# Performance work log

Hardware: AMD Instinct MI355X
Metric: run time of the kernel (lower is better)

The kernel has to match this reference:

```python
import jax, jax.numpy as jnp
import numpy as np

B, C, N, DI, DC = 64, 32, 1152, 8, 16
ROUTINGS = 3


def squash(x, axis=-1):
    sq = jnp.sum(x * x, axis=axis, keepdims=True)
    scale = sq / (1.0 + sq) / jnp.sqrt(sq + 1e-07)
    return scale * x


def setup_inputs() -> dict:
    key = jax.random.key(0)
    k1, k2 = jax.random.split(key)
    inputs = jax.random.normal(k1, (B, N, DI), dtype=jnp.float32)
    # Xavier-uniform init for W[n_caps, n_in, d_cap, d_in]; fan computed over last two dims
    limit = float(np.sqrt(6.0 / (DC + DI)))
    W = jax.random.uniform(k2, (C, N, DC, DI), dtype=jnp.float32, minval=-limit, maxval=limit)
    return {"inputs": inputs, "W": W}


def reference(inputs, W):
    # inputs_hat[b,c,n,i] = sum_j W[c,n,i,j] * inputs[b,n,j]
    inputs_hat = jnp.einsum('cnij,bnj->bcni', W, inputs)  # [B,C,N,DC]
    b = jnp.zeros((B, C, N), dtype=inputs_hat.dtype)
    outputs = None
    for i in range(ROUTINGS):
        c = jax.nn.softmax(b, axis=1)                      # over output capsules
        s = jnp.einsum('bcn,bcni->bci', c, inputs_hat)     # weighted sum over input caps
        outputs = squash(s)                                # [B,C,DC]
        if i < ROUTINGS - 1:
            agreement = jnp.einsum('bci,bcni->bcn', outputs, inputs_hat)
            b = b + agreement
    return outputs
```

## Files before the change

kernel.cpp:

```cpp
#include <hip/hip_runtime.h>
#include <hip/hip_bf16.h>
#include <hip/hip_fp16.h>

#define B_  64
#define C_  32
#define N_  1152
#define DI_ 8
#define DC_ 16
#define NCH 3
#define NSLOT 128
#define STH 512
#define NOCT 16

static __device__ __forceinline__ unsigned pkh(float a, float b) {
    __half2 t = __float22half2_rn(make_float2(a, b));
    return *reinterpret_cast<unsigned*>(&t);
}
static __device__ __forceinline__ float2 uph(unsigned u) {
    __half2 h; *reinterpret_cast<unsigned*>(&h) = u;
    return __half22float2(h);
}

__global__ __launch_bounds__(STH, 4) void caps_hat(
    const float* __restrict__ X, const float* __restrict__ W,
    uint4* __restrict__ hatg, float* __restrict__ p1)
{
    __shared__ float wlds[NCH * 64 * 64];
    __shared__ float xlds[NCH * 16 * 8];

    const int xcd  = blockIdx.x & 7;
    const int j    = blockIdx.x >> 3;
    const int slot = xcd * 16 + (j & 15);
    const int bg   = j >> 4;

    const int tid  = threadIdx.x;
    const int w    = tid >> 6;
    const int lane = tid & 63;
    const int c    = lane & 31;
    const int h    = lane >> 5;
    const int bl0  = w * 2;
    const int le   = 2 * c + h;
    const int sw   = c & 7;

    float acc[2][8];
#pragma unroll
    for (int bq = 0; bq < 2; bq++)
#pragma unroll
        for (int r = 0; r < 8; r++) acc[bq][r] = 0.f;

    for (int cc = 0; cc < 3; cc++) {
        if (cc) __syncthreads();
        const int n0 = (slot + cc * NSLOT) * NCH;

        for (int G = tid; G < NCH * 1024; G += STH) {
            const int nl = G >> 10, f = (G >> 4) & 63, q = G & 15;
            const int wc = f >> 1, wh = f & 1;
            const float4 v = *(const float4*)(W + (size_t)(wc * N_ + n0 + nl) * 128 + wh * 64 + q * 4);
            *(float4*)(wlds + (nl * 64 + f) * 64 + (q ^ (wc & 7)) * 4) = v;
        }
        if (tid < NCH * 32) {
            const int nl = tid >> 5, bl = (tid >> 1) & 15, qx = tid & 1;
            const float4 v = *(const float4*)(X + (size_t)((bg * 16 + bl) * N_ + n0 + nl) * DI_ + qx * 4);
            *(float4*)(xlds + (nl * 16 + bl) * 8 + qx * 4) = v;
        }
        __syncthreads();

#pragma unroll
        for (int nl = 0; nl < NCH; nl++) {
            float4 xa[2], xb[2];
#pragma unroll
            for (int bq = 0; bq < 2; bq++) {
                const float* xp = xlds + (nl * 16 + bl0 + bq) * 8;
                xa[bq] = *(const float4*)xp;
                xb[bq] = *(const float4*)(xp + 4);
            }
            uint4 hq[2];
            const float* frag = wlds + (nl * 64 + le) * 64;
#pragma unroll
            for (int rp = 0; rp < 4; rp++) {
                const int r0 = 2 * rp, r1 = r0 + 1;
                const int pa0 = ((2 * r0) ^ sw) * 4;
                const int pb0 = pa0 ^ 4;
                const int pa1 = ((2 * r1) ^ sw) * 4;
                const int pb1 = pa1 ^ 4;
                const float4 wa0 = *(const float4*)(frag + pa0);
                const float4 wb0 = *(const float4*)(frag + pb0);
                const float4 wa1 = *(const float4*)(frag + pa1);
                const float4 wb1 = *(const float4*)(frag + pb1);
#pragma unroll
                for (int bq = 0; bq < 2; bq++) {
                    const float hv0 = wa0.x*xa[bq].x + wa0.y*xa[bq].y + wa0.z*xa[bq].z + wa0.w*xa[bq].w
                                    + wb0.x*xb[bq].x + wb0.y*xb[bq].y + wb0.z*xb[bq].z + wb0.w*xb[bq].w;
                    const float hv1 = wa1.x*xa[bq].x + wa1.y*xa[bq].y + wa1.z*xa[bq].z + wa1.w*xa[bq].w
                                    + wb1.x*xb[bq].x + wb1.y*xb[bq].y + wb1.z*xb[bq].z + wb1.w*xb[bq].w;
                    acc[bq][r0] += hv0;
                    acc[bq][r1] += hv1;
                    (&hq[bq].x)[rp] = pkh(hv0, hv1);
                }
            }
#pragma unroll
            for (int bq = 0; bq < 2; bq++) {
                const int b = bg * 16 + bl0 + bq;
                hatg[(size_t)(b * N_ + n0 + nl) * 64 + le] = hq[bq];
            }
        }
    }

    float* pout = p1 + (size_t)(bg * NSLOT + slot) * (16 * 512);
#pragma unroll
    for (int bq = 0; bq < 2; bq++) {
        float* pb = pout + (bl0 + bq) * 512 + le * 8;
        *(float4*)pb       = make_float4(acc[bq][0]*0.03125f, acc[bq][1]*0.03125f,
                                         acc[bq][2]*0.03125f, acc[bq][3]*0.03125f);
        *(float4*)(pb + 4) = make_float4(acc[bq][4]*0.03125f, acc[bq][5]*0.03125f,
                                         acc[bq][6]*0.03125f, acc[bq][7]*0.03125f);
    }
}

__global__ __launch_bounds__(STH, 2) void caps_route(
    const uint4* __restrict__ hatg, const float* __restrict__ accb,
    float* __restrict__ p2)
{
    __shared__ float red[8 * 512];
    const int b    = blockIdx.x >> 4;
    const int oct  = blockIdx.x & 15;
    const int tid  = threadIdx.x;
    const int w    = tid >> 6;
    const int lane = tid & 63;
    const int c    = lane & 31;
    const int h    = lane >> 5;
    const int le   = 2 * c + h;

    const float* ap = accb + (size_t)b * 512 + le * 8;
    const float4 a0 = *(const float4*)ap;
    const float4 a1 = *(const float4*)(ap + 4);

    const uint4* hb = hatg + (size_t)(b * N_ + oct * 72) * 64 + le;

    uint4 v[9];
#pragma unroll
    for (int m = 0; m < 9; m++)
        v[m] = hb[(size_t)(w + 8 * m) * 64];

    float lg[9], sm[9];
#pragma unroll
    for (int m = 0; m < 9; m++) {
        const float2 f0 = uph(v[m].x);
        const float2 f1 = uph(v[m].y);
        const float2 f2 = uph(v[m].z);
        const float2 f3 = uph(v[m].w);
        lg[m] = f0.x*a0.x + f0.y*a0.y + f1.x*a0.z + f1.y*a0.w
              + f2.x*a1.x + f2.y*a1.y + f3.x*a1.z + f3.y*a1.w;
    }
#pragma unroll
    for (int m = 0; m < 9; m++) lg[m] += __shfl_xor(lg[m], 32, 64);
#pragma unroll
    for (int m = 0; m < 9; m++) { lg[m] = __expf(lg[m]); sm[m] = lg[m]; }
#pragma unroll
    for (int d = 16; d >= 1; d >>= 1)
#pragma unroll
        for (int m = 0; m < 9; m++) sm[m] += __shfl_xor(sm[m], d, 64);

    float acc[8] = {0.f,0.f,0.f,0.f,0.f,0.f,0.f,0.f};
#pragma unroll
    for (int m = 0; m < 9; m++) {
        const float sc = lg[m] * __builtin_amdgcn_rcpf(sm[m]);
        const float2 f0 = uph(v[m].x);
        const float2 f1 = uph(v[m].y);
        const float2 f2 = uph(v[m].z);
        const float2 f3 = uph(v[m].w);
        acc[0] += sc * f0.x; acc[1] += sc * f0.y;
        acc[2] += sc * f1.x; acc[3] += sc * f1.y;
        acc[4] += sc * f2.x; acc[5] += sc * f2.y;
        acc[6] += sc * f3.x; acc[7] += sc * f3.y;
    }
    *(float4*)(red + w * 512 + le * 8)     = make_float4(acc[0], acc[1], acc[2], acc[3]);
    *(float4*)(red + w * 512 + le * 8 + 4) = make_float4(acc[4], acc[5], acc[6], acc[7]);
    __syncthreads();
    float vs = 0.f;
#pragma unroll
    for (int s = 0; s < 8; s++) vs += red[s * 512 + tid];
    p2[(size_t)(b * NOCT + oct) * 512 + tid] = vs;
}

__global__ __launch_bounds__(512) void caps_r1(
    const float* __restrict__ p1, float* __restrict__ accb,
    float* __restrict__ out, int t)
{
    const int b   = blockIdx.x >> 2;
    const int q   = blockIdx.x & 3;
    const int tid = threadIdx.x;
    const int e   = q * 128 + (tid >> 2);
    const int p   = tid & 3;
    const int bg  = b >> 4, bl = b & 15;
    const float* base = p1 + (size_t)bg * NSLOT * 8192 + (size_t)bl * 512 + e;
    float v = 0.f;
#pragma unroll 8
    for (int ch = p; ch < NSLOT; ch += 4)
        v += base[(size_t)ch * 8192];
    v += __shfl_xor(v, 1, 64);
    v += __shfl_xor(v, 2, 64);
    float sq = v * v;
#pragma unroll
    for (int m = 4; m <= 32; m <<= 1) sq += __shfl_xor(sq, m, 64);
    const float scale = sq / (1.f + sq) * rsqrtf(sq + 1e-7f);
    const float ov = v * scale;
    if (p == 0) {
        const int oidx = b * 512 + e;
        if (t == 2) out[oidx] = ov;
        else        accb[oidx] = (t == 0) ? ov : (accb[oidx] + ov);
    }
}

__global__ __launch_bounds__(512) void caps_r2(
    const float* __restrict__ p2, float* __restrict__ accb,
    float* __restrict__ out, int t)
{
    const int b = blockIdx.x;
    const int e = threadIdx.x;
    const float* base = p2 + (size_t)b * (NOCT * 512) + e;
    float v = 0.f;
#pragma unroll
    for (int s = 0; s < NOCT; s++) v += base[s * 512];
    float sq = v * v;
#pragma unroll
    for (int m = 1; m <= 8; m <<= 1) sq += __shfl_xor(sq, m, 64);
    const float scale = sq / (1.f + sq) * rsqrtf(sq + 1e-7f);
    const float ov = v * scale;
    const int oidx = b * 512 + e;
    if (t == 2) out[oidx] = ov;
    else        accb[oidx] += ov;
}

__global__ __launch_bounds__(STH, 2) void caps_s_fb(
    const float* __restrict__ X, const float* __restrict__ W,
    const float* __restrict__ aout, float* __restrict__ partials, int t)
{
    __shared__ float wlds[NCH * 64 * 64];
    __shared__ float xlds[NCH * 16 * 8];
    const int bg = blockIdx.x & 3, slot = blockIdx.x >> 2;
    const int tid = threadIdx.x, w = tid >> 6, lane = tid & 63;
    const int c = lane & 31, h = lane >> 5, bl0 = w * 2, sw = c & 7;
    float areg[2][8] = {};
    if (t > 0) {
#pragma unroll
        for (int bq = 0; bq < 2; bq++) {
            const float* ap = aout + (size_t)(bg * 16 + bl0 + bq) * 512 + c * 16 + h * 8;
            const float4 a0 = *(const float4*)ap; const float4 a1 = *(const float4*)(ap + 4);
            areg[bq][0]=a0.x; areg[bq][1]=a0.y; areg[bq][2]=a0.z; areg[bq][3]=a0.w;
            areg[bq][4]=a1.x; areg[bq][5]=a1.y; areg[bq][6]=a1.z; areg[bq][7]=a1.w;
        }
    }
    float acc[2][8];
#pragma unroll
    for (int bq = 0; bq < 2; bq++)
#pragma unroll
        for (int r = 0; r < 8; r++) acc[bq][r] = 0.f;
    for (int cc = 0; cc < 3; cc++) {
        if (cc) __syncthreads();
        const int n0 = (slot + cc * NSLOT) * NCH;
        for (int G = tid; G < NCH * 1024; G += STH) {
            const int nl = G >> 10, f = (G >> 4) & 63, q = G & 15;
            const int wc = f >> 1, wh = f & 1;
            const float4 v = *(const float4*)(W + (size_t)(wc * N_ + n0 + nl) * 128 + wh * 64 + q * 4);
            *(float4*)(wlds + (nl * 64 + f) * 64 + (q ^ (wc & 7)) * 4) = v;
        }
        if (tid < NCH * 32) {
            const int nl = tid >> 5, bl = (tid >> 1) & 15, qx = tid & 1;
            const float4 v = *(const float4*)(X + (size_t)((bg * 16 + bl) * N_ + n0 + nl) * DI_ + qx * 4);
            *(float4*)(xlds + (nl * 16 + bl) * 8 + qx * 4) = v;
        }
        __syncthreads();
#pragma unroll
        for (int nl = 0; nl < NCH; nl++) {
            float4 xa[2], xb[2];
#pragma unroll
            for (int bq = 0; bq < 2; bq++) {
                const float* xp = xlds + (nl * 16 + bl0 + bq) * 8;
                xa[bq] = *(const float4*)xp; xb[bq] = *(const float4*)(xp + 4);
            }
            float hat[2][8];
            const float* frag = wlds + (nl * 64 + 2 * c + h) * 64;
#pragma unroll
            for (int r = 0; r < 8; r++) {
                const int pa = ((2 * r) ^ sw) * 4; const int pb = pa ^ 4;
                const float4 wa = *(const float4*)(frag + pa);
                const float4 wb = *(const float4*)(frag + pb);
#pragma unroll
                for (int bq = 0; bq < 2; bq++)
                    hat[bq][r] = wa.x*xa[bq].x + wa.y*xa[bq].y + wa.z*xa[bq].z + wa.w*xa[bq].w
                               + wb.x*xb[bq].x + wb.y*xb[bq].y + wb.z*xb[bq].z + wb.w*xb[bq].w;
            }
#pragma unroll
            for (int bq = 0; bq < 2; bq++) {
                float softc;
                if (t > 0) {
                    float lg = hat[bq][0]*areg[bq][0] + hat[bq][1]*areg[bq][1]
                             + hat[bq][2]*areg[bq][2] + hat[bq][3]*areg[bq][3]
                             + hat[bq][4]*areg[bq][4] + hat[bq][5]*areg[bq][5]
                             + hat[bq][6]*areg[bq][6] + hat[bq][7]*areg[bq][7];
                    lg += __shfl_xor(lg, 32, 64);
                    const float e = __expf(lg);
                    float s = e;
#pragma unroll
                    for (int m = 16; m >= 1; m >>= 1) s += __shfl_xor(s, m, 64);
                    softc = e / s;
                } else softc = 1.0f / 32.0f;
#pragma unroll
                for (int r = 0; r < 8; r++) acc[bq][r] += softc * hat[bq][r];
            }
        }
    }
    float* pout = partials + (size_t)(bg * NSLOT + slot) * (16 * 512);
#pragma unroll
    for (int bq = 0; bq < 2; bq++) {
        float* pb = pout + (bl0 + bq) * 512 + c * 16 + h * 8;
        *(float4*)pb       = make_float4(acc[bq][0], acc[bq][1], acc[bq][2], acc[bq][3]);
        *(float4*)(pb + 4) = make_float4(acc[bq][4], acc[bq][5], acc[bq][6], acc[bq][7]);
    }
}

__global__ __launch_bounds__(256) void caps_r1_fb(
    const float* __restrict__ partials, float* __restrict__ accb,
    float* __restrict__ out, int t)
{
    const int b   = blockIdx.x >> 2;
    const int q   = blockIdx.x & 3;
    const int tid = threadIdx.x;
    const int e   = q * 128 + (tid >> 1);
    const int p   = tid & 1;
    const int bg  = b >> 4, bl = b & 15;
    const float* base = partials + (size_t)bg * NSLOT * 8192 + (size_t)bl * 512 + e;
    float v = 0.f;
#pragma unroll 8
    for (int ch = p; ch < NSLOT; ch += 2)
        v += base[(size_t)ch * 8192];
    v += __shfl_xor(v, 1, 64);
    float sq = v * v;
#pragma unroll
    for (int m = 2; m <= 16; m <<= 1) sq += __shfl_xor(sq, m, 64);
    const float scale = sq / (1.f + sq) * rsqrtf(sq + 1e-7f);
    const float ov = v * scale;
    if (p == 0) {
        const int oidx = b * 512 + e;
        if (t == 2) out[oidx] = ov;
        else        accb[oidx] = (t == 0) ? ov : (accb[oidx] + ov);
    }
}

extern "C" void kernel_launch(void* const* d_in, const int* in_sizes, int n_in,
                              void* d_out, int out_size, void* d_ws, size_t ws_size,
                              hipStream_t stream) {
    const float* X = (const float*)d_in[0];
    const float* W = (const float*)d_in[1];
    float* out = (float*)d_out;

    const size_t hat_b = (size_t)B_ * N_ * 512 * 2;
    const size_t p1_b  = (size_t)512 * 8192 * 4;
    const size_t p2_b  = (size_t)B_ * NOCT * 512 * 4;
    const size_t acc_b = (size_t)B_ * 512 * 4;

    if (ws_size >= hat_b + p1_b + p2_b + acc_b) {
        char* ws = (char*)d_ws;
        uint4* hatg = (uint4*)ws;
        float* p1   = (float*)(ws + hat_b);
        float* p2   = (float*)(ws + hat_b + p1_b);
        float* accb = (float*)(ws + hat_b + p1_b + p2_b);
        caps_hat  <<<512, STH, 0, stream>>>(X, W, hatg, p1);
        caps_r1   <<<256, 512, 0, stream>>>(p1, accb, out, 0);
        caps_route<<<B_ * NOCT, STH, 0, stream>>>(hatg, accb, p2);
        caps_r2   <<<64, 512, 0, stream>>>(p2, accb, out, 1);
        caps_route<<<B_ * NOCT, STH, 0, stream>>>(hatg, accb, p2);
        caps_r2   <<<64, 512, 0, stream>>>(p2, accb, out, 2);
    } else {
        float* partials = (float*)d_ws;
        float* accb = partials + (size_t)512 * 8192;
        for (int t = 0; t < 3; t++) {
            caps_s_fb<<<512, STH, 0, stream>>>(X, W, accb, partials, t);
            caps_r1_fb<<<256, 256, 0, stream>>>(partials, accb, out, t);
        }
    }
}
```

Before: 125.9 us.

## Rebalance capsule hat and routing grids, read inputs directly from global

The hat kernel now processes 2 input capsules per chunk over 192 slots, launching 768 blocks instead of 512. It drops the shared-memory staging of X in favour of direct global loads. The routing kernel splits the N dimension into 24 pieces of 48 instead of 16 of 72, uses an XCD-aware block mapping, and raises its occupancy hint. The aim is more blocks for better CU fill and lower LDS use, at the cost of more partial sums for the reducers (caps_r1 over 192 slots, caps_r2 over 24 pieces) and redundant X loads across waves.

```diff
diff --git a/kernel.cpp b/kernel.cpp
--- a/kernel.cpp
+++ b/kernel.cpp
@@ -7,10 +7,14 @@
 #define N_  1152
 #define DI_ 8
 #define DC_ 16
-#define NCH 3
-#define NSLOT 128
 #define STH 512
-#define NOCT 16
+
+#define HCH 2
+#define HSLOT 192
+#define NOCT 24
+
+#define FCH 3
+#define FSLOT 128
 
 static __device__ __forceinline__ unsigned pkh(float a, float b) {
     __half2 t = __float22half2_rn(make_float2(a, b));
@@ -25,22 +29,21 @@
     const float* __restrict__ X, const float* __restrict__ W,
     uint4* __restrict__ hatg, float* __restrict__ p1)
 {
-    __shared__ float wlds[NCH * 64 * 64];
-    __shared__ float xlds[NCH * 16 * 8];
+    __shared__ float wlds[HCH * 64 * 64];
 
     const int xcd  = blockIdx.x & 7;
-    const int j    = blockIdx.x >> 3;
-    const int slot = xcd * 16 + (j & 15);
-    const int bg   = j >> 4;
+    const int k    = blockIdx.x >> 3;
+    const int bg   = k & 3;
+    const int slot = 24 * xcd + (k >> 2);
 
     const int tid  = threadIdx.x;
-    const int w    = tid >> 6;
     const int lane = tid & 63;
     const int c    = lane & 31;
     const int h    = lane >> 5;
-    const int bl0  = w * 2;
     const int le   = 2 * c + h;
     const int sw   = c & 7;
+    const int wu   = __builtin_amdgcn_readfirstlane(tid) >> 6;
+    const int bl0  = wu * 2;
 
     float acc[2][8];
 #pragma unroll
@@ -50,27 +53,23 @@
 
     for (int cc = 0; cc < 3; cc++) {
         if (cc) __syncthreads();
-        const int n0 = (slot + cc * NSLOT) * NCH;
-
-        for (int G = tid; G < NCH * 1024; G += STH) {
+        const int n0 = (slot + cc * HSLOT) * HCH;
+
+#pragma unroll
+        for (int G = tid; G < HCH * 1024; G += STH) {
             const int nl = G >> 10, f = (G >> 4) & 63, q = G & 15;
             const int wc = f >> 1, wh = f & 1;
             const float4 v = *(const float4*)(W + (size_t)(wc * N_ + n0 + nl) * 128 + wh * 64 + q * 4);
             *(float4*)(wlds + (nl * 64 + f) * 64 + (q ^ (wc & 7)) * 4) = v;
         }
-        if (tid < NCH * 32) {
-            const int nl = tid >> 5, bl = (tid >> 1) & 15, qx = tid & 1;
-            const float4 v = *(const float4*)(X + (size_t)((bg * 16 + bl) * N_ + n0 + nl) * DI_ + qx * 4);
-            *(float4*)(xlds + (nl * 16 + bl) * 8 + qx * 4) = v;
-        }
         __syncthreads();
 
 #pragma unroll
-        for (int nl = 0; nl < NCH; nl++) {
+        for (int nl = 0; nl < HCH; nl++) {
             float4 xa[2], xb[2];
 #pragma unroll
             for (int bq = 0; bq < 2; bq++) {
-                const float* xp = xlds + (nl * 16 + bl0 + bq) * 8;
+                const float* xp = X + ((size_t)(bg * 16 + bl0 + bq) * N_ + n0 + nl) * DI_;
                 xa[bq] = *(const float4*)xp;
                 xb[bq] = *(const float4*)(xp + 4);
             }
@@ -106,7 +105,7 @@
         }
     }
 
-    float* pout = p1 + (size_t)(bg * NSLOT + slot) * (16 * 512);
+    float* pout = p1 + (size_t)(bg * HSLOT + slot) * (16 * 512);
 #pragma unroll
     for (int bq = 0; bq < 2; bq++) {
         float* pb = pout + (bl0 + bq) * 512 + le * 8;
@@ -117,13 +116,16 @@
     }
 }
 
-__global__ __launch_bounds__(STH, 2) void caps_route(
+__global__ __launch_bounds__(STH, 4) void caps_route(
     const uint4* __restrict__ hatg, const float* __restrict__ accb,
     float* __restrict__ p2)
 {
     __shared__ float red[8 * 512];
-    const int b    = blockIdx.x >> 4;
-    const int oct  = blockIdx.x & 15;
+    const int xcd  = blockIdx.x & 7;
+    const int rest = blockIdx.x >> 3;
+    const int ug   = rest % 3;
+    const int b    = rest / 3;
+    const int u    = 8 * ug + xcd;
     const int tid  = threadIdx.x;
     const int w    = tid >> 6;
     const int lane = tid & 63;
@@ -135,16 +137,16 @@
     const float4 a0 = *(const float4*)ap;
     const float4 a1 = *(const float4*)(ap + 4);
 
-    const uint4* hb = hatg + (size_t)(b * N_ + oct * 72) * 64 + le;
-
-    uint4 v[9];
-#pragma unroll
-    for (int m = 0; m < 9; m++)
+    const uint4* hb = hatg + (size_t)(b * N_ + u * 48) * 64 + le;
+
+    uint4 v[6];
+#pragma unroll
+    for (int m = 0; m < 6; m++)
         v[m] = hb[(size_t)(w + 8 * m) * 64];
 
-    float lg[9], sm[9];
-#pragma unroll
-    for (int m = 0; m < 9; m++) {
+    float lg[6], sm[6];
+#pragma unroll
+    for (int m = 0; m < 6; m++) {
         const float2 f0 = uph(v[m].x);
         const float2 f1 = uph(v[m].y);
         const float2 f2 = uph(v[m].z);
@@ -153,17 +155,17 @@
               + f2.x*a1.x + f2.y*a1.y + f3.x*a1.z + f3.y*a1.w;
     }
 #pragma unroll
-    for (int m = 0; m < 9; m++) lg[m] += __shfl_xor(lg[m], 32, 64);
-#pragma unroll
-    for (int m = 0; m < 9; m++) { lg[m] = __expf(lg[m]); sm[m] = lg[m]; }
+    for (int m = 0; m < 6; m++) lg[m] += __shfl_xor(lg[m], 32, 64);
+#pragma unroll
+    for (int m = 0; m < 6; m++) { lg[m] = __expf(lg[m]); sm[m] = lg[m]; }
 #pragma unroll
     for (int d = 16; d >= 1; d >>= 1)
 #pragma unroll
-        for (int m = 0; m < 9; m++) sm[m] += __shfl_xor(sm[m], d, 64);
+        for (int m = 0; m < 6; m++) sm[m] += __shfl_xor(sm[m], d, 64);
 
     float acc[8] = {0.f,0.f,0.f,0.f,0.f,0.f,0.f,0.f};
 #pragma unroll
-    for (int m = 0; m < 9; m++) {
+    for (int m = 0; m < 6; m++) {
         const float sc = lg[m] * __builtin_amdgcn_rcpf(sm[m]);
         const float2 f0 = uph(v[m].x);
         const float2 f1 = uph(v[m].y);
@@ -180,7 +182,7 @@
     float vs = 0.f;
 #pragma unroll
     for (int s = 0; s < 8; s++) vs += red[s * 512 + tid];
-    p2[(size_t)(b * NOCT + oct) * 512 + tid] = vs;
+    p2[(size_t)(b * NOCT + u) * 512 + tid] = vs;
 }
 
 __global__ __launch_bounds__(512) void caps_r1(
@@ -193,10 +195,10 @@
     const int e   = q * 128 + (tid >> 2);
     const int p   = tid & 3;
     const int bg  = b >> 4, bl = b & 15;
-    const float* base = p1 + (size_t)bg * NSLOT * 8192 + (size_t)bl * 512 + e;
+    const float* base = p1 + (size_t)bg * HSLOT * 8192 + (size_t)bl * 512 + e;
     float v = 0.f;
 #pragma unroll 8
-    for (int ch = p; ch < NSLOT; ch += 4)
+    for (int ch = p; ch < HSLOT; ch += 4)
         v += base[(size_t)ch * 8192];
     v += __shfl_xor(v, 1, 64);
     v += __shfl_xor(v, 2, 64);
@@ -236,8 +238,8 @@
     const float* __restrict__ X, const float* __restrict__ W,
     const float* __restrict__ aout, float* __restrict__ partials, int t)
 {
-    __shared__ float wlds[NCH * 64 * 64];
-    __shared__ float xlds[NCH * 16 * 8];
+    __shared__ float wlds[FCH * 64 * 64];
+    __shared__ float xlds[FCH * 16 * 8];
     const int bg = blockIdx.x & 3, slot = blockIdx.x >> 2;
     const int tid = threadIdx.x, w = tid >> 6, lane = tid & 63;
     const int c = lane & 31, h = lane >> 5, bl0 = w * 2, sw = c & 7;
@@ -258,21 +260,21 @@
         for (int r = 0; r < 8; r++) acc[bq][r] = 0.f;
     for (int cc = 0; cc < 3; cc++) {
         if (cc) __syncthreads();
-        const int n0 = (slot + cc * NSLOT) * NCH;
-        for (int G = tid; G < NCH * 1024; G += STH) {
+        const int n0 = (slot + cc * FSLOT) * FCH;
+        for (int G = tid; G < FCH * 1024; G += STH) {
             const int nl = G >> 10, f = (G >> 4) & 63, q = G & 15;
             const int wc = f >> 1, wh = f & 1;
             const float4 v = *(const float4*)(W + (size_t)(wc * N_ + n0 + nl) * 128 + wh * 64 + q * 4);
             *(float4*)(wlds + (nl * 64 + f) * 64 + (q ^ (wc & 7)) * 4) = v;
         }
-        if (tid < NCH * 32) {
+        if (tid < FCH * 32) {
             const int nl = tid >> 5, bl = (tid >> 1) & 15, qx = tid & 1;
             const float4 v = *(const float4*)(X + (size_t)((bg * 16 + bl) * N_ + n0 + nl) * DI_ + qx * 4);
             *(float4*)(xlds + (nl * 16 + bl) * 8 + qx * 4) = v;
         }
         __syncthreads();
 #pragma unroll
-        for (int nl = 0; nl < NCH; nl++) {
+        for (int nl = 0; nl < FCH; nl++) {
             float4 xa[2], xb[2];
 #pragma unroll
             for (int bq = 0; bq < 2; bq++) {
@@ -311,7 +313,7 @@
             }
         }
     }
-    float* pout = partials + (size_t)(bg * NSLOT + slot) * (16 * 512);
+    float* pout = partials + (size_t)(bg * FSLOT + slot) * (16 * 512);
 #pragma unroll
     for (int bq = 0; bq < 2; bq++) {
         float* pb = pout + (bl0 + bq) * 512 + c * 16 + h * 8;
@@ -330,10 +332,10 @@
     const int e   = q * 128 + (tid >> 1);
     const int p   = tid & 1;
     const int bg  = b >> 4, bl = b & 15;
-    const float* base = partials + (size_t)bg * NSLOT * 8192 + (size_t)bl * 512 + e;
+    const float* base = partials + (size_t)bg * FSLOT * 8192 + (size_t)bl * 512 + e;
     float v = 0.f;
 #pragma unroll 8
-    for (int ch = p; ch < NSLOT; ch += 2)
+    for (int ch = p; ch < FSLOT; ch += 2)
         v += base[(size_t)ch * 8192];
     v += __shfl_xor(v, 1, 64);
     float sq = v * v;
@@ -356,7 +358,7 @@
     float* out = (float*)d_out;
 
     const size_t hat_b = (size_t)B_ * N_ * 512 * 2;
-    const size_t p1_b  = (size_t)512 * 8192 * 4;
+    const size_t p1_b  = (size_t)4 * HSLOT * 8192 * 4;
     const size_t p2_b  = (size_t)B_ * NOCT * 512 * 4;
     const size_t acc_b = (size_t)B_ * 512 * 4;
 
@@ -366,7 +368,7 @@
         float* p1   = (float*)(ws + hat_b);
         float* p2   = (float*)(ws + hat_b + p1_b);
         float* accb = (float*)(ws + hat_b + p1_b + p2_b);
-        caps_hat  <<<512, STH, 0, stream>>>(X, W, hatg, p1);
+        caps_hat  <<<768, STH, 0, stream>>>(X, W, hatg, p1);
         caps_r1   <<<256, 512, 0, stream>>>(p1, accb, out, 0);
         caps_route<<<B_ * NOCT, STH, 0, stream>>>(hatg, accb, p2);
         caps_r2   <<<64, 512, 0, stream>>>(p2, accb, out, 1);
```

Result: slower. 128.9 us (+2.3%).
